# Kernel optimization log

Measured on AMD Instinct MI355X. Metric: run time of the kernel, lower is better.

Reference implementation:

```python
import jax, jax.numpy as jnp
import numpy as np


def setup_inputs() -> dict:
    key = jax.random.key(0)
    k1, k2 = jax.random.split(key)
    pred = jax.random.normal(k1, (16, 4096, 3), dtype=jnp.float32)
    target = jax.random.normal(k2, (16, 4096, 3), dtype=jnp.float32)
    return {"pred": pred, "target": target}


def _pairwise_l2(pc1, pc2):
    # pc1: (B,N,3), pc2: (B,M,3) -> (B,N,M) euclidean distances (torch.cdist p=2)
    sq1 = jnp.sum(pc1 * pc1, axis=-1)  # (B,N)
    sq2 = jnp.sum(pc2 * pc2, axis=-1)  # (B,M)
    inner = jnp.einsum("bnd,bmd->bnm", pc1, pc2)  # (B,N,M)
    d2 = sq1[:, :, None] + sq2[:, None, :] - 2.0 * inner
    return jnp.sqrt(jnp.maximum(d2, 0.0))


def reference(pred, target):
    d = _pairwise_l2(pred, target)          # (B,N,M)
    dist1 = jnp.mean(jnp.min(d, axis=2), axis=1)  # (B,) pred -> target
    dist2 = jnp.mean(jnp.min(d, axis=1), axis=1)  # (B,) target -> pred
    chamfer = (dist1 + dist2) / 2.0         # bidirectional=True
    return jnp.mean(chamfer)
```

## Files before the change

### kernel.cpp

```cpp
#include <hip/hip_runtime.h>
#include <math.h>
#include <stdint.h>


#define BATCH   16
#define NPTS    4096
#define THREADS 256
#define NITEMS  (2 * BATCH * NPTS)
#define MAIN_BLOCKS (2 * BATCH * (NPTS / 128))

typedef __attribute__((ext_vector_type(8)))  _Float16 half8;
typedef __attribute__((ext_vector_type(16))) float    floatx16;

union Pack16 { float4 f4; _Float16 h[8]; half8 h8; };

__global__ __launch_bounds__(256) void chamfer_prep(
    const float* __restrict__ pred, const float* __restrict__ target,
    float4* __restrict__ packP, float4* __restrict__ packT)
{
    int g = blockIdx.x * 256 + threadIdx.x;
    int arr = g >> 16;
    int pt  = g & 65535;
    const float* src = arr ? target : pred;
    float x = src[pt * 3 + 0];
    float y = src[pt * 3 + 1];
    float z = src[pt * 3 + 2];
    _Float16 hx = (_Float16)x, hy = (_Float16)y, hz = (_Float16)z;
    float xf = (float)hx, yf = (float)hy, zf = (float)hz;
    float t = xf * xf + yf * yf + zf * zf;
    _Float16 h1 = (_Float16)t;
    _Float16 h2 = (_Float16)(t - (float)h1);
    Pack16 p;
    p.h[0] = hx; p.h[1] = hy; p.h[2] = hz; p.h[3] = h1; p.h[4] = h2;
    p.h[5] = (_Float16)0.0f; p.h[6] = (_Float16)0.0f; p.h[7] = (_Float16)0.0f;
    (arr ? packT : packP)[pt] = p.f4;
}

__device__ inline half8 make_bfrag(const Pack16& praw, bool lo) {
    half8 f;
#pragma unroll
    for (int i = 0; i < 8; ++i) f[i] = (_Float16)0.0f;
    if (lo) {
        f[0] = (_Float16)(praw.h[0] * (_Float16)-2.0f);
        f[1] = (_Float16)(praw.h[1] * (_Float16)-2.0f);
        f[2] = (_Float16)(praw.h[2] * (_Float16)-2.0f);
        f[3] = (_Float16)1.0f;
        f[4] = (_Float16)1.0f;
    }
    return f;
}

__global__ __launch_bounds__(THREADS, 4) void chamfer_main(
    const float4* __restrict__ packP, const float4* __restrict__ packT,
    float* __restrict__ blocksum)
{
    __shared__ float pmin[4][64];
    __shared__ float wsum[2];

    int tid  = threadIdx.x;
    int lane = tid & 63;
    int wave = tid >> 6;
    int qhalf = wave & 1;
    int chalf = wave >> 1;
    int l31  = lane & 31;
    bool lo  = lane < 32;

    int id = blockIdx.x;
    int ng = id & 31; id >>= 5;
    int b  = id & 15; id >>= 4;
    int dir = id;

    const float4* qpack = dir ? packT : packP;
    const float4* cpack = dir ? packP : packT;

    size_t qbase = (size_t)b * NPTS + ng * 128 + qhalf * 64;
    Pack16 prA, prB;
    prA.f4 = qpack[qbase + l31];
    prB.f4 = qpack[qbase + 32 + l31];
    half8 bfragA = make_bfrag(prA, lo);
    half8 bfragB = make_bfrag(prB, lo);

    const float4* cb = cpack + (size_t)b * NPTS + chalf * 2048;

    floatx16 zero, mnA, mnB;
#pragma unroll
    for (int r = 0; r < 16; ++r) { zero[r] = 0.0f; mnA[r] = 1e30f; mnB[r] = 1e30f; }

#pragma unroll 2
    for (int t = 0; t < 32; ++t) {
        Pack16 a0, a1;
        a0.f4 = cb[t * 64 + l31];
        a1.f4 = cb[t * 64 + 32 + l31];
        floatx16 d0 = __builtin_amdgcn_mfma_f32_32x32x16_f16(a0.h8, bfragA, zero, 0, 0, 0);
        floatx16 d1 = __builtin_amdgcn_mfma_f32_32x32x16_f16(a0.h8, bfragB, zero, 0, 0, 0);
#pragma unroll
        for (int r = 0; r < 16; ++r) mnA[r] = fminf(d0[r], mnA[r]);
#pragma unroll
        for (int r = 0; r < 16; ++r) mnB[r] = fminf(d1[r], mnB[r]);
        floatx16 d2 = __builtin_amdgcn_mfma_f32_32x32x16_f16(a1.h8, bfragA, zero, 0, 0, 0);
        floatx16 d3 = __builtin_amdgcn_mfma_f32_32x32x16_f16(a1.h8, bfragB, zero, 0, 0, 0);
#pragma unroll
        for (int r = 0; r < 16; ++r) mnA[r] = fminf(d2[r], mnA[r]);
#pragma unroll
        for (int r = 0; r < 16; ++r) mnB[r] = fminf(d3[r], mnB[r]);
    }

    float mA = fminf(fminf(fminf(mnA[0], mnA[1]),   fminf(mnA[2], mnA[3])),
                     fminf(fminf(mnA[4], mnA[5]),   fminf(mnA[6], mnA[7])));
    mA = fminf(mA, fminf(fminf(fminf(mnA[8], mnA[9]),   fminf(mnA[10], mnA[11])),
                         fminf(fminf(mnA[12], mnA[13]), fminf(mnA[14], mnA[15]))));
    float mB = fminf(fminf(fminf(mnB[0], mnB[1]),   fminf(mnB[2], mnB[3])),
                     fminf(fminf(mnB[4], mnB[5]),   fminf(mnB[6], mnB[7])));
    mB = fminf(mB, fminf(fminf(fminf(mnB[8], mnB[9]),   fminf(mnB[10], mnB[11])),
                         fminf(fminf(mnB[12], mnB[13]), fminf(mnB[14], mnB[15]))));
    mA = fminf(mA, __shfl_xor(mA, 32));
    mB = fminf(mB, __shfl_xor(mB, 32));
    if (lo) {
        pmin[wave][l31]      = mA;
        pmin[wave][l31 + 32] = mB;
    }
    __syncthreads();

    if (wave < 2) {
        float mm = fminf(pmin[wave][lane], pmin[wave + 2][lane]);
        Pack16 pr;
        pr.f4 = qpack[(size_t)b * NPTS + ng * 128 + wave * 64 + lane];
        float psq = (float)pr.h[3] + (float)pr.h[4];
        float dist = sqrtf(fmaxf(mm + psq, 0.0f));
#pragma unroll
        for (int off = 1; off <= 32; off <<= 1)
            dist += __shfl_xor(dist, off);
        if (lane == 0) wsum[wave] = dist;
    }
    __syncthreads();

    if (tid == 0)
        blocksum[blockIdx.x] = wsum[0] + wsum[1];
}

__global__ __launch_bounds__(256) void chamfer_finish(
    const float4* __restrict__ bs, float* __restrict__ out)
{
    __shared__ float ws[4];
    int tid = threadIdx.x;
    float4 v = bs[tid];
    float s = (v.x + v.y) + (v.z + v.w);
#pragma unroll
    for (int off = 1; off <= 32; off <<= 1)
        s += __shfl_xor(s, off);
    int lane = tid & 63, wave = tid >> 6;
    if (lane == 0) ws[wave] = s;
    __syncthreads();
    if (tid == 0) out[0] = (ws[0] + ws[1] + ws[2] + ws[3]) * (1.0f / (float)NITEMS);
}

extern "C" void kernel_launch(void* const* d_in, const int* in_sizes, int n_in,
                              void* d_out, int out_size, void* d_ws, size_t ws_size,
                              hipStream_t stream) {
    const float* pred   = (const float*)d_in[0];
    const float* target = (const float*)d_in[1];
    float* out = (float*)d_out;

    float4* packP = (float4*)d_ws;
    float4* packT = packP + (size_t)BATCH * NPTS;
    float*  blocksum = (float*)(packT + (size_t)BATCH * NPTS);

    chamfer_prep<<<NITEMS / 256, 256, 0, stream>>>(pred, target, packP, packT);
    chamfer_main<<<MAIN_BLOCKS, THREADS, 0, stream>>>(packP, packT, blocksum);
    chamfer_finish<<<1, 256, 0, stream>>>((const float4*)blocksum, out);
}
```

Measured before the change: 76.02 us.

## Fuse point packing into main kernel via shared-memory candidate slabs

Removes the separate prep kernel. Each block now reads raw fp32 points, packs the candidate set into fp16 float4 records in LDS in two slabs of 2048, and packs its own query points in registers. This saves one kernel launch and the workspace round trip. The cost is redundant packing work: each of the 32 blocks per batch and direction repacks all 4096 candidates. It also adds 32KB of LDS per block and extra barriers, which may limit occupancy under launch_bounds(256,4).

```diff
diff --git a/kernel.cpp b/kernel.cpp
--- a/kernel.cpp
+++ b/kernel.cpp
@@ -8,23 +8,14 @@
 #define THREADS 256
 #define NITEMS  (2 * BATCH * NPTS)
 #define MAIN_BLOCKS (2 * BATCH * (NPTS / 128))
+#define SLAB    2048
 
 typedef __attribute__((ext_vector_type(8)))  _Float16 half8;
 typedef __attribute__((ext_vector_type(16))) float    floatx16;
 
 union Pack16 { float4 f4; _Float16 h[8]; half8 h8; };
 
-__global__ __launch_bounds__(256) void chamfer_prep(
-    const float* __restrict__ pred, const float* __restrict__ target,
-    float4* __restrict__ packP, float4* __restrict__ packT)
-{
-    int g = blockIdx.x * 256 + threadIdx.x;
-    int arr = g >> 16;
-    int pt  = g & 65535;
-    const float* src = arr ? target : pred;
-    float x = src[pt * 3 + 0];
-    float y = src[pt * 3 + 1];
-    float z = src[pt * 3 + 2];
+__device__ inline Pack16 pack_point(float x, float y, float z) {
     _Float16 hx = (_Float16)x, hy = (_Float16)y, hz = (_Float16)z;
     float xf = (float)hx, yf = (float)hy, zf = (float)hz;
     float t = xf * xf + yf * yf + zf * zf;
@@ -33,7 +24,7 @@
     Pack16 p;
     p.h[0] = hx; p.h[1] = hy; p.h[2] = hz; p.h[3] = h1; p.h[4] = h2;
     p.h[5] = (_Float16)0.0f; p.h[6] = (_Float16)0.0f; p.h[7] = (_Float16)0.0f;
-    (arr ? packT : packP)[pt] = p.f4;
+    return p;
 }
 
 __device__ inline half8 make_bfrag(const Pack16& praw, bool lo) {
@@ -51,9 +42,10 @@
 }
 
 __global__ __launch_bounds__(THREADS, 4) void chamfer_main(
-    const float4* __restrict__ packP, const float4* __restrict__ packT,
+    const float* __restrict__ pred, const float* __restrict__ target,
     float* __restrict__ blocksum)
 {
+    __shared__ __align__(16) float4 cbuf[SLAB];
     __shared__ float pmin[4][64];
     __shared__ float wsum[2];
 
@@ -70,39 +62,47 @@
     int b  = id & 15; id >>= 4;
     int dir = id;
 
-    const float4* qpack = dir ? packT : packP;
-    const float4* cpack = dir ? packP : packT;
+    const float* qsrc = (dir ? target : pred) + (size_t)b * (NPTS * 3);
+    const float* csrc = (dir ? pred : target) + (size_t)b * (NPTS * 3);
 
-    size_t qbase = (size_t)b * NPTS + ng * 128 + qhalf * 64;
-    Pack16 prA, prB;
-    prA.f4 = qpack[qbase + l31];
-    prB.f4 = qpack[qbase + 32 + l31];
+    int q0 = ng * 128 + qhalf * 64 + l31;
+    Pack16 prA = pack_point(qsrc[q0 * 3], qsrc[q0 * 3 + 1], qsrc[q0 * 3 + 2]);
+    Pack16 prB = pack_point(qsrc[(q0 + 32) * 3], qsrc[(q0 + 32) * 3 + 1], qsrc[(q0 + 32) * 3 + 2]);
     half8 bfragA = make_bfrag(prA, lo);
     half8 bfragB = make_bfrag(prB, lo);
-
-    const float4* cb = cpack + (size_t)b * NPTS + chalf * 2048;
 
     floatx16 zero, mnA, mnB;
 #pragma unroll
     for (int r = 0; r < 16; ++r) { zero[r] = 0.0f; mnA[r] = 1e30f; mnB[r] = 1e30f; }
 
+    for (int pass = 0; pass < 2; ++pass) {
+        __syncthreads();
+#pragma unroll
+        for (int i = tid; i < SLAB; i += THREADS) {
+            int c = pass * SLAB + i;
+            cbuf[i] = pack_point(csrc[c * 3], csrc[c * 3 + 1], csrc[c * 3 + 2]).f4;
+        }
+        __syncthreads();
+
+        const float4* cb = &cbuf[chalf * 1024];
 #pragma unroll 2
-    for (int t = 0; t < 32; ++t) {
-        Pack16 a0, a1;
-        a0.f4 = cb[t * 64 + l31];
-        a1.f4 = cb[t * 64 + 32 + l31];
-        floatx16 d0 = __builtin_amdgcn_mfma_f32_32x32x16_f16(a0.h8, bfragA, zero, 0, 0, 0);
-        floatx16 d1 = __builtin_amdgcn_mfma_f32_32x32x16_f16(a0.h8, bfragB, zero, 0, 0, 0);
+        for (int t = 0; t < 16; ++t) {
+            Pack16 a0, a1;
+            a0.f4 = cb[t * 64 + l31];
+            a1.f4 = cb[t * 64 + 32 + l31];
+            floatx16 d0 = __builtin_amdgcn_mfma_f32_32x32x16_f16(a0.h8, bfragA, zero, 0, 0, 0);
+            floatx16 d1 = __builtin_amdgcn_mfma_f32_32x32x16_f16(a0.h8, bfragB, zero, 0, 0, 0);
 #pragma unroll
-        for (int r = 0; r < 16; ++r) mnA[r] = fminf(d0[r], mnA[r]);
+            for (int r = 0; r < 16; ++r) mnA[r] = fminf(d0[r], mnA[r]);
 #pragma unroll
-        for (int r = 0; r < 16; ++r) mnB[r] = fminf(d1[r], mnB[r]);
-        floatx16 d2 = __builtin_amdgcn_mfma_f32_32x32x16_f16(a1.h8, bfragA, zero, 0, 0, 0);
-        floatx16 d3 = __builtin_amdgcn_mfma_f32_32x32x16_f16(a1.h8, bfragB, zero, 0, 0, 0);
+            for (int r = 0; r < 16; ++r) mnB[r] = fminf(d1[r], mnB[r]);
+            floatx16 d2 = __builtin_amdgcn_mfma_f32_32x32x16_f16(a1.h8, bfragA, zero, 0, 0, 0);
+            floatx16 d3 = __builtin_amdgcn_mfma_f32_32x32x16_f16(a1.h8, bfragB, zero, 0, 0, 0);
 #pragma unroll
-        for (int r = 0; r < 16; ++r) mnA[r] = fminf(d2[r], mnA[r]);
+            for (int r = 0; r < 16; ++r) mnA[r] = fminf(d2[r], mnA[r]);
 #pragma unroll
-        for (int r = 0; r < 16; ++r) mnB[r] = fminf(d3[r], mnB[r]);
+            for (int r = 0; r < 16; ++r) mnB[r] = fminf(d3[r], mnB[r]);
+        }
     }
 
     float mA = fminf(fminf(fminf(mnA[0], mnA[1]),   fminf(mnA[2], mnA[3])),
@@ -123,8 +123,8 @@
 
     if (wave < 2) {
         float mm = fminf(pmin[wave][lane], pmin[wave + 2][lane]);
-        Pack16 pr;
-        pr.f4 = qpack[(size_t)b * NPTS + ng * 128 + wave * 64 + lane];
+        int q = ng * 128 + wave * 64 + lane;
+        Pack16 pr = pack_point(qsrc[q * 3], qsrc[q * 3 + 1], qsrc[q * 3 + 2]);
         float psq = (float)pr.h[3] + (float)pr.h[4];
         float dist = sqrtf(fmaxf(mm + psq, 0.0f));
 #pragma unroll
@@ -161,11 +161,8 @@
     const float* target = (const float*)d_in[1];
     float* out = (float*)d_out;
 
-    float4* packP = (float4*)d_ws;
-    float4* packT = packP + (size_t)BATCH * NPTS;
-    float*  blocksum = (float*)(packT + (size_t)BATCH * NPTS);
+    float* blocksum = (float*)d_ws;
 
-    chamfer_prep<<<NITEMS / 256, 256, 0, stream>>>(pred, target, packP, packT);
-    chamfer_main<<<MAIN_BLOCKS, THREADS, 0, stream>>>(packP, packT, blocksum);
+    chamfer_main<<<MAIN_BLOCKS, THREADS, 0, stream>>>(pred, target, blocksum);
     chamfer_finish<<<1, 256, 0, stream>>>((const float4*)blocksum, out);
 }
```

Measured after the change: 80.04 us. +5.3%, slower.
